# Kernel tuning notes

Hardware: AMD Instinct MI355X
Metric: run time of the kernel (lower is better)

Reference implementation:

```python
import jax, jax.numpy as jnp
import numpy as np

D_MODEL = 1024
N_HEADS = 16
HEAD_DIM = D_MODEL // N_HEADS
WINDOW = 512


def _rope(q, k, seq_len, head_dim):
    # interleaved RoPE, identical to the torch implementation
    theta = 1.0 / 10000.0 ** (jnp.arange(0, head_dim, 2, dtype=jnp.float32) / head_dim)
    pos = jnp.arange(seq_len, dtype=jnp.float32)
    freqs = jnp.outer(pos, theta)                      # [S, hD/2]
    cos_f = jnp.cos(freqs)[None, None]                 # [1,1,S,hD/2]
    sin_f = jnp.sin(freqs)[None, None]

    def rotate(x):
        x1, x2 = x[..., ::2], x[..., 1::2]
        return jnp.stack([x1 * cos_f - x2 * sin_f, x1 * sin_f + x2 * cos_f], axis=-1).reshape(x.shape)

    return rotate(q), rotate(k)


def _sliding_window_attn(q, k, v, W, scale):
    # chunked O(S*W) causal sliding-window attention
    B, nH, S, hD = q.shape
    n_chunks = (S + W - 1) // W
    pad_s = n_chunks * W - S
    k_pad = jnp.pad(k, ((0, 0), (0, 0), (W, pad_s), (0, 0)))
    v_pad = jnp.pad(v, ((0, 0), (0, 0), (W, pad_s), (0, 0)))
    q_pad = jnp.pad(q, ((0, 0), (0, 0), (0, pad_s), (0, 0)))
    q_c = q_pad.reshape(B, nH, n_chunks, W, hD)
    k_r = k_pad.reshape(B, nH, n_chunks + 1, W, hD)
    v_r = v_pad.reshape(B, nH, n_chunks + 1, W, hD)
    # window i = chunks [i, i+1] of the left-padded sequence (== torch unfold)
    k_c = jnp.concatenate([k_r[:, :, :-1], k_r[:, :, 1:]], axis=3)  # [B,nH,C,2W,hD]
    v_c = jnp.concatenate([v_r[:, :, :-1], v_r[:, :, 1:]], axis=3)
    attn = jnp.einsum('bhcqd,bhckd->bhcqk', q_c, k_c) * scale

    qi = jnp.arange(W)[:, None]
    ki = jnp.arange(2 * W)[None, :]
    cw_mask = (ki <= qi) | (ki > qi + W)               # [W, 2W]
    chunk_idx = jnp.arange(n_chunks)[:, None]
    abs_k = chunk_idx * W + ki - W                     # [C, 2W]
    pad_mask = (abs_k < 0) | (abs_k >= S)
    q_pos = jnp.arange(n_chunks * W).reshape(n_chunks, W)
    full_mask = cw_mask[None] | pad_mask[:, None, :] | (q_pos >= S)[..., None]  # [C,W,2W]

    attn = jnp.where(full_mask[None, None], -jnp.inf, attn)
    attn = jax.nn.softmax(attn, axis=-1)
    attn = jnp.nan_to_num(attn, nan=0.0)
    out = jnp.einsum('bhcqk,bhckd->bhcqd', attn, v_c)
    return out.reshape(B, nH, n_chunks * W, hD)[:, :, :S]


def _rmsnorm(x, w):
    eps = jnp.finfo(x.dtype).eps
    return x * jax.lax.rsqrt(jnp.mean(x * x, axis=-1, keepdims=True) + eps) * w


def _sdpa(q, k, v, scale):
    s = jnp.einsum('bhqd,bhkd->bhqk', q, k) * scale
    return jnp.einsum('bhqk,bhkd->bhqd', jax.nn.softmax(s, axis=-1), v)


def setup_inputs() -> dict:
    key = jax.random.key(0)
    ks = jax.random.split(key, 11)
    D = D_MODEL
    std = 0.02
    return {
        'x': jax.random.normal(ks[0], (2, 4096, D), jnp.float32),
        'landmarks': jax.random.normal(ks[1], (2, 256, D), jnp.float32),
        'archived_landmarks': jax.random.normal(ks[2], (2, 128, D), jnp.float32),
        'W_qkv': jax.random.normal(ks[3], (D, 3 * D), jnp.float32) * std,
        'W_lm': jax.random.normal(ks[4], (D, 2 * D), jnp.float32) * std,
        'W_arch': jax.random.normal(ks[5], (D, 2 * D), jnp.float32) * std,
        'W_o': jax.random.normal(ks[6], (D, D), jnp.float32) * std,
        'W_gate': jax.random.normal(ks[7], (3 * D, 2 * D), jnp.float32) * std,
        'g_local': jnp.ones((D,), jnp.float32),
        'g_lm': jnp.ones((D,), jnp.float32),
        'g_arch': jnp.ones((D,), jnp.float32),
    }


def reference(x, landmarks, archived_landmarks, W_qkv, W_lm, W_arch, W_o, W_gate, g_local, g_lm, g_arch):
    B, S, D = x.shape
    nH, hD = N_HEADS, HEAD_DIM
    scale = hD ** -0.5

    def rsh(t, L):
        return jnp.transpose(t.reshape(B, L, nH, hD), (0, 2, 1, 3))

    q, k, v = jnp.split(x @ W_qkv, 3, axis=-1)
    Q, K, V = rsh(q, S), rsh(k, S), rsh(v, S)
    Q, K = _rope(Q, K, S, hD)

    Weff = min(WINDOW, S)
    out_loc = _sliding_window_attn(Q, K, V, Weff, scale)  # S > Weff -> chunked path
    out_loc = _rmsnorm(jnp.transpose(out_loc, (0, 2, 1, 3)).reshape(B, S, D), g_local)

    L = landmarks.shape[1]
    K_lm, V_lm = jnp.split(landmarks @ W_lm, 2, axis=-1)
    out_lm = _sdpa(Q, rsh(K_lm, L), rsh(V_lm, L), scale)
    out_lm = _rmsnorm(jnp.transpose(out_lm, (0, 2, 1, 3)).reshape(B, S, D), g_lm)

    A = archived_landmarks.shape[1]
    K_a, V_a = jnp.split(archived_landmarks @ W_arch, 2, axis=-1)
    out_a = _sdpa(Q, rsh(K_a, A), rsh(V_a, A), scale)
    out_a = _rmsnorm(jnp.transpose(out_a, (0, 2, 1, 3)).reshape(B, S, D), g_arch)

    concat = jnp.concatenate([out_loc, out_lm, out_a], axis=-1)
    gate, value = jnp.split(concat @ W_gate, 2, axis=-1)
    return (jax.nn.silu(gate) * value) @ W_o
```

## Files before the change

kernel.cpp:

```cpp
#include <hip/hip_runtime.h>
#include <cstdint>
#include <cstddef>

typedef __bf16 bf16;
typedef __bf16 bf16x2 __attribute__((ext_vector_type(2)));
typedef __bf16 bf16x4 __attribute__((ext_vector_type(4)));
typedef __bf16 bf16x8 __attribute__((ext_vector_type(8)));
typedef float  f32x2 __attribute__((ext_vector_type(2)));
typedef float  f32x4 __attribute__((ext_vector_type(4)));

#define DEVFN __device__ __forceinline__

DEVFN void gld_lds16(void* lds, const void* g) {
  __builtin_amdgcn_global_load_lds(
      (__attribute__((address_space(1))) void*)g,
      (__attribute__((address_space(3))) void*)lds,
      16, 0, 0);
}

__global__ void cast_f32_bf16(const float* __restrict__ in, bf16* __restrict__ out, int n4) {
  int i = blockIdx.x * blockDim.x + threadIdx.x;
  if (i < n4) {
    f32x4 v = reinterpret_cast<const f32x4*>(in)[i];
    bf16x4 o;
    o[0] = (bf16)v[0]; o[1] = (bf16)v[1]; o[2] = (bf16)v[2]; o[3] = (bf16)v[3];
    reinterpret_cast<bf16x4*>(out)[i] = o;
  }
}

__global__ void transpose_cast(const float* __restrict__ in, bf16* __restrict__ out,
                               int R, int C) {
  __shared__ float t[32][33];
  int tx = threadIdx.x, ty = threadIdx.y;
  int c = blockIdx.x * 32 + tx;
  #pragma unroll
  for (int j = 0; j < 4; ++j) {
    int r = blockIdx.y * 32 + ty + j * 8;
    t[ty + j * 8][tx] = in[(size_t)r * C + c];
  }
  __syncthreads();
  int rr = blockIdx.y * 32 + tx;
  #pragma unroll
  for (int j = 0; j < 4; ++j) {
    int cc = blockIdx.x * 32 + ty + j * 8;
    out[(size_t)cc * R + rr] = (bf16)t[tx][ty + j * 8];
  }
}

__global__ void rope_table(float* __restrict__ tab) {
  int idx = blockIdx.x * 256 + threadIdx.x;
  int s = idx >> 5, i = idx & 31;
  float theta = powf(10000.f, -(float)(2 * i) * (1.f / 64.f));
  float f = (float)s * theta;
  tab[idx * 2]     = cosf(f);
  tab[idx * 2 + 1] = sinf(f);
}

template<typename OT>
__global__ __launch_bounds__(256) void gemm_bf16(
    const bf16* __restrict__ A, const bf16* __restrict__ Bt, OT* __restrict__ C,
    int M, int N, int K) {
  __shared__ alignas(16) bf16 As[128 * 64];
  __shared__ alignas(16) bf16 Bs[128 * 64];
  int tid = threadIdx.x;
  int w = tid >> 6, l = tid & 63;
  int l15 = l & 15, lg = l >> 4;
  int m0 = blockIdx.y * 128;
  int n0 = blockIdx.x * 128;
  int wr = (w >> 1) * 64, wc = (w & 1) * 64;
  f32x4 acc[4][4] = {};
  const size_t aBase = (size_t)m0 * K;
  const size_t bBase = (size_t)n0 * K;
  int nk = K >> 6;
  for (int kt = 0; kt < nk; ++kt) {
    int k0 = kt << 6;
    #pragma unroll
    for (int it = 0; it < 4; ++it) {
      int c = it * 256 + tid;
      int row = c >> 3, c8 = c & 7;
      gld_lds16(&As[(size_t)(it * 256 + w * 64) * 8],
                A + aBase + (size_t)row * K + k0 + c8 * 8);
      gld_lds16(&Bs[(size_t)(it * 256 + w * 64) * 8],
                Bt + bBase + (size_t)row * K + k0 + c8 * 8);
    }
    __syncthreads();
    #pragma unroll
    for (int kk = 0; kk < 64; kk += 32) {
      bf16x8 a[4], b[4];
      #pragma unroll
      for (int i = 0; i < 4; ++i)
        a[i] = *reinterpret_cast<const bf16x8*>(&As[(wr + i * 16 + l15) * 64 + kk + lg * 8]);
      #pragma unroll
      for (int i = 0; i < 4; ++i)
        b[i] = *reinterpret_cast<const bf16x8*>(&Bs[(wc + i * 16 + l15) * 64 + kk + lg * 8]);
      #pragma unroll
      for (int mi = 0; mi < 4; ++mi)
        #pragma unroll
        for (int ni = 0; ni < 4; ++ni)
          acc[mi][ni] = __builtin_amdgcn_mfma_f32_16x16x32_bf16(a[mi], b[ni], acc[mi][ni], 0, 0, 0);
    }
    __syncthreads();
  }
  #pragma unroll
  for (int mi = 0; mi < 4; ++mi) {
    #pragma unroll
    for (int r = 0; r < 4; ++r) {
      int row = m0 + wr + mi * 16 + lg * 4 + r;
      OT* crow = C + (size_t)row * N + n0 + wc + l15;
      #pragma unroll
      for (int ni = 0; ni < 4; ++ni) crow[ni * 16] = (OT)acc[mi][ni][r];
    }
  }
}

__global__ void rope_qk(const bf16* __restrict__ qkv, const float* __restrict__ tab,
                        bf16* __restrict__ Qb, bf16* __restrict__ Kb) {
  int idx = blockIdx.x * 256 + threadIdx.x;
  int i = idx & 31;
  int h = (idx >> 5) & 15;
  int bs = idx >> 9;
  int s = bs & 4095;
  int b = bs >> 12;
  const bf16* row = qkv + (size_t)bs * 3072;
  bf16x2 q2 = *reinterpret_cast<const bf16x2*>(row + h * 64 + 2 * i);
  bf16x2 k2 = *reinterpret_cast<const bf16x2*>(row + 1024 + h * 64 + 2 * i);
  f32x2 cs = *reinterpret_cast<const f32x2*>(tab + s * 64 + 2 * i);
  float c = cs[0], sn = cs[1];
  float q0 = (float)q2[0], q1 = (float)q2[1];
  float k0 = (float)k2[0], k1 = (float)k2[1];
  size_t ob = (((size_t)(b * 16 + h) * 4096) + s) * 64 + 2 * i;
  bf16x2 qo, ko;
  qo[0] = (bf16)((q0 * c - q1 * sn) * 0.125f);
  qo[1] = (bf16)((q0 * sn + q1 * c) * 0.125f);
  ko[0] = (bf16)(k0 * c - k1 * sn);
  ko[1] = (bf16)(k0 * sn + k1 * c);
  *reinterpret_cast<bf16x2*>(Qb + ob) = qo;
  *reinterpret_cast<bf16x2*>(Kb + ob) = ko;
}

__global__ void kv_post(const bf16* __restrict__ kv, bf16* __restrict__ Kdst,
                        bf16* __restrict__ Vt, int Lk, int rs, int koff, int voff) {
  __shared__ float t[64][65];
  int s0 = blockIdx.x * 64;
  int h = blockIdx.y, b = blockIdx.z;
  int tid = threadIdx.x;
  int lane_d = tid & 63;
  int rq = tid >> 6;
  const bf16* base = kv + (size_t)b * Lk * rs;
  if (Kdst) {
    #pragma unroll
    for (int r = 0; r < 16; ++r) {
      int si = r * 4 + rq;
      Kdst[(((size_t)(b * 16 + h) * Lk) + s0 + si) * 64 + lane_d] =
          base[(size_t)(s0 + si) * rs + koff + h * 64 + lane_d];
    }
  }
  #pragma unroll
  for (int r = 0; r < 16; ++r) {
    int si = r * 4 + rq;
    t[si][lane_d] = (float)base[(size_t)(s0 + si) * rs + voff + h * 64 + lane_d];
  }
  __syncthreads();
  #pragma unroll
  for (int r = 0; r < 16; ++r) {
    int d = r * 4 + rq;
    Vt[(((size_t)(b * 16 + h) * 64) + d) * Lk + s0 + lane_d] = (bf16)t[lane_d][d];
  }
}

template<bool WINDOWED>
__global__ __launch_bounds__(256) void attn_kernel(
    const bf16* __restrict__ Qb, const bf16* __restrict__ Kb, const bf16* __restrict__ Vt,
    bf16* __restrict__ outc, int S, int Lk, int col_off) {
  __shared__ alignas(16) bf16 Ks[64 * 64];
  __shared__ alignas(16) bf16 Vs[64 * 64];
  __shared__ alignas(16) bf16 Ps[4][16 * 72];
  int tid = threadIdx.x;
  int w = tid >> 6, l = tid & 63;
  int l15 = l & 15, lg = l >> 4;
  int qt = blockIdx.x, h = blockIdx.y, b = blockIdx.z;

  size_t qrow = (((size_t)(b * 16 + h) * S) + qt * 64 + w * 16 + l15) * 64;
  bf16x8 qf[2];
  qf[0] = *reinterpret_cast<const bf16x8*>(Qb + qrow + lg * 8);
  qf[1] = *reinterpret_cast<const bf16x8*>(Qb + qrow + 32 + lg * 8);
  const bf16* Kbase = Kb + ((size_t)(b * 16 + h) * Lk) * 64;
  const bf16* Vbase = Vt + ((size_t)(b * 16 + h) * 64) * Lk;

  float mrow = -1e30f, lsum = 0.f;
  f32x4 acc[4] = {};

  int kt_hi, kt_lo;
  if (WINDOWED) { kt_hi = qt; kt_lo = qt >= 8 ? qt - 8 : 0; }
  else          { kt_hi = (Lk >> 6) - 1; kt_lo = 0; }

  for (int kt = kt_hi; kt >= kt_lo; --kt) {
    const bf16* kg = Kbase + (size_t)kt * 64 * 64;
    #pragma unroll
    for (int it = 0; it < 2; ++it)
      gld_lds16(&Ks[(it * 256 + w * 64) * 8], kg + (size_t)(it * 256 + tid) * 8);
    #pragma unroll
    for (int it = 0; it < 2; ++it) {
      int c = it * 256 + tid;
      int row = c >> 3, c8 = c & 7;
      gld_lds16(&Vs[(it * 256 + w * 64) * 8],
                Vbase + (size_t)row * Lk + kt * 64 + c8 * 8);
    }
    __syncthreads();

    f32x4 st[4] = {};
    #pragma unroll
    for (int kk = 0; kk < 2; ++kk) {
      #pragma unroll
      for (int f = 0; f < 4; ++f) {
        bf16x8 kf = *reinterpret_cast<const bf16x8*>(&Ks[(f * 16 + l15) * 64 + kk * 32 + lg * 8]);
        st[f] = __builtin_amdgcn_mfma_f32_16x16x32_bf16(kf, qf[kk], st[f], 0, 0, 0);
      }
    }

    if (WINDOWED) {
      int qi = w * 16 + l15;
      if (kt == qt) {
        #pragma unroll
        for (int f = 0; f < 4; ++f)
          #pragma unroll
          for (int r = 0; r < 4; ++r)
            if (f * 16 + lg * 4 + r > qi) st[f][r] = -1e30f;
      } else if (kt == qt - 8) {
        #pragma unroll
        for (int f = 0; f < 4; ++f)
          #pragma unroll
          for (int r = 0; r < 4; ++r)
            if (f * 16 + lg * 4 + r <= qi) st[f][r] = -1e30f;
      }
    }

    float rm = -1e30f;
    #pragma unroll
    for (int f = 0; f < 4; ++f)
      #pragma unroll
      for (int r = 0; r < 4; ++r) rm = fmaxf(rm, st[f][r]);
    rm = fmaxf(rm, __shfl_xor(rm, 16));
    rm = fmaxf(rm, __shfl_xor(rm, 32));
    float mnew = fmaxf(mrow, rm);
    float fsc = __expf(mrow - mnew);
    float ps = 0.f;
    bf16x4 pv[4];
    #pragma unroll
    for (int f = 0; f < 4; ++f)
      #pragma unroll
      for (int r = 0; r < 4; ++r) {
        float p = __expf(st[f][r] - mnew);
        ps += p;
        pv[f][r] = (bf16)p;
      }
    ps += __shfl_xor(ps, 16);
    ps += __shfl_xor(ps, 32);
    lsum = lsum * fsc + ps;
    mrow = mnew;

    #pragma unroll
    for (int f = 0; f < 4; ++f)
      *reinterpret_cast<bf16x4*>(&Ps[w][l15 * 72 + f * 16 + lg * 4]) = pv[f];

    #pragma unroll
    for (int r = 0; r < 4; ++r) {
      float fr = __shfl(fsc, lg * 4 + r);
      #pragma unroll
      for (int f = 0; f < 4; ++f) acc[f][r] *= fr;
    }

    #pragma unroll
    for (int kk = 0; kk < 2; ++kk) {
      bf16x8 pa = *reinterpret_cast<const bf16x8*>(&Ps[w][l15 * 72 + kk * 32 + lg * 8]);
      #pragma unroll
      for (int f = 0; f < 4; ++f) {
        bf16x8 vf = *reinterpret_cast<const bf16x8*>(&Vs[(f * 16 + l15) * 64 + kk * 32 + lg * 8]);
        acc[f] = __builtin_amdgcn_mfma_f32_16x16x32_bf16(pa, vf, acc[f], 0, 0, 0);
      }
    }
    __syncthreads();
  }

  float inv = 1.f / lsum;
  #pragma unroll
  for (int r = 0; r < 4; ++r) {
    float ir = __shfl(inv, lg * 4 + r);
    int srow = qt * 64 + w * 16 + lg * 4 + r;
    bf16* orow = outc + ((size_t)b * S + srow) * 3072 + col_off + h * 64 + l15;
    #pragma unroll
    for (int f = 0; f < 4; ++f) orow[f * 16] = (bf16)(acc[f][r] * ir);
  }
}

__global__ __launch_bounds__(256) void rmsnorm_kernel(
    bf16* data, const float* __restrict__ g0,
    const float* __restrict__ g1, const float* __restrict__ g2) {
  int token = blockIdx.x;
  int seg = blockIdx.y;
  const float* g = seg == 0 ? g0 : (seg == 1 ? g1 : g2);
  int tid = threadIdx.x;
  size_t base = (size_t)token * 3072 + seg * 1024;
  bf16x4 bv = reinterpret_cast<const bf16x4*>(data + base)[tid];
  f32x4 v;
  #pragma unroll
  for (int j = 0; j < 4; ++j) v[j] = (float)bv[j];
  float ss = v[0] * v[0] + v[1] * v[1] + v[2] * v[2] + v[3] * v[3];
  #pragma unroll
  for (int m = 1; m < 64; m <<= 1) ss += __shfl_xor(ss, m);
  __shared__ float red[4];
  if ((tid & 63) == 0) red[tid >> 6] = ss;
  __syncthreads();
  float tot = red[0] + red[1] + red[2] + red[3];
  float sc = rsqrtf(tot * (1.f / 1024.f) + 1.19209290e-07f);
  f32x4 gv = reinterpret_cast<const f32x4*>(g)[tid];
  bf16x4 o;
  #pragma unroll
  for (int j = 0; j < 4; ++j) o[j] = (bf16)(v[j] * sc * gv[j]);
  reinterpret_cast<bf16x4*>(data + base)[tid] = o;
}

__global__ void silu_kernel(const bf16* __restrict__ gv, bf16* __restrict__ out) {
  int T = blockIdx.x * 256 + threadIdx.x;
  int row = T >> 8, c4 = (T & 255) * 4;
  bf16x4 g = *reinterpret_cast<const bf16x4*>(gv + (size_t)row * 2048 + c4);
  bf16x4 vv = *reinterpret_cast<const bf16x4*>(gv + (size_t)row * 2048 + 1024 + c4);
  bf16x4 o;
  #pragma unroll
  for (int j = 0; j < 4; ++j) {
    float x = (float)g[j];
    o[j] = (bf16)((x / (1.f + __expf(-x))) * (float)vv[j]);
  }
  *reinterpret_cast<bf16x4*>(out + (size_t)row * 1024 + c4) = o;
}

extern "C" void kernel_launch(void* const* d_in, const int* in_sizes, int n_in,
                              void* d_out, int out_size, void* d_ws, size_t ws_size,
                              hipStream_t stream) {
  (void)in_sizes; (void)n_in; (void)out_size; (void)ws_size;
  const float* x       = (const float*)d_in[0];
  const float* lm      = (const float*)d_in[1];
  const float* arch    = (const float*)d_in[2];
  const float* W_qkv   = (const float*)d_in[3];
  const float* W_lm    = (const float*)d_in[4];
  const float* W_arch  = (const float*)d_in[5];
  const float* W_o     = (const float*)d_in[6];
  const float* W_gate  = (const float*)d_in[7];
  const float* g_local = (const float*)d_in[8];
  const float* g_lm    = (const float*)d_in[9];
  const float* g_arch  = (const float*)d_in[10];
  float* out = (float*)d_out;

  char* ws = (char*)d_ws;
  size_t off = 0;
  auto alloc = [&](size_t bytes) -> void* {
    void* p = ws + off;
    off += (bytes + 255) & ~(size_t)255;
    return p;
  };
  bf16*  Wqkv_t   = (bf16*) alloc(3072ull * 1024 * 2);
  bf16*  Wlm_t    = (bf16*) alloc(2048ull * 1024 * 2);
  bf16*  Warch_t  = (bf16*) alloc(2048ull * 1024 * 2);
  bf16*  Wgate_t  = (bf16*) alloc(2048ull * 3072 * 2);
  bf16*  Wo_t     = (bf16*) alloc(1024ull * 1024 * 2);
  bf16*  lm_bf    = (bf16*) alloc(512ull * 1024 * 2);
  bf16*  arch_bf  = (bf16*) alloc(256ull * 1024 * 2);
  float* ropetab  = (float*)alloc(4096ull * 64 * 4);
  bf16*  Klm      = (bf16*) alloc(2ull * 16 * 256 * 64 * 2);
  bf16*  Vlm_t    = (bf16*) alloc(2ull * 16 * 64 * 256 * 2);
  bf16*  Ka       = (bf16*) alloc(2ull * 16 * 128 * 64 * 2);
  bf16*  Va_t     = (bf16*) alloc(2ull * 16 * 64 * 128 * 2);
  bf16*  lmkv_bf  = (bf16*) alloc(512ull * 2048 * 2);
  bf16*  akv_bf   = (bf16*) alloc(256ull * 2048 * 2);
  char* R1 = (char*)alloc(8192ull * 1024 * 2);
  bf16* x_bf  = (bf16*)R1;
  bf16* gated = (bf16*)R1;
  char* R2 = (char*)alloc(8192ull * 3072 * 2);
  bf16* qkv_bf  = (bf16*)R2;
  bf16* concatb = (bf16*)R2;
  char* R3 = (char*)alloc(3ull * 16 * 1024 * 1024);
  bf16* Qb = (bf16*)R3;
  bf16* Kb = (bf16*)(R3 + 16ull * 1024 * 1024);
  bf16* Vt = (bf16*)(R3 + 32ull * 1024 * 1024);
  bf16* gv = (bf16*)R3;

  transpose_cast<<<dim3(96, 32), dim3(32, 8), 0, stream>>>(W_qkv, Wqkv_t, 1024, 3072);
  transpose_cast<<<dim3(64, 32), dim3(32, 8), 0, stream>>>(W_lm, Wlm_t, 1024, 2048);
  transpose_cast<<<dim3(64, 32), dim3(32, 8), 0, stream>>>(W_arch, Warch_t, 1024, 2048);
  transpose_cast<<<dim3(64, 96), dim3(32, 8), 0, stream>>>(W_gate, Wgate_t, 3072, 2048);
  transpose_cast<<<dim3(32, 32), dim3(32, 8), 0, stream>>>(W_o, Wo_t, 1024, 1024);
  cast_f32_bf16<<<8192, 256, 0, stream>>>(x, x_bf, 8192 * 1024 / 4);
  cast_f32_bf16<<<512, 256, 0, stream>>>(lm, lm_bf, 512 * 1024 / 4);
  cast_f32_bf16<<<256, 256, 0, stream>>>(arch, arch_bf, 256 * 1024 / 4);
  rope_table<<<512, 256, 0, stream>>>(ropetab);

  gemm_bf16<bf16><<<dim3(24, 64), 256, 0, stream>>>(x_bf, Wqkv_t, qkv_bf, 8192, 3072, 1024);
  gemm_bf16<bf16><<<dim3(16, 4), 256, 0, stream>>>(lm_bf, Wlm_t, lmkv_bf, 512, 2048, 1024);
  gemm_bf16<bf16><<<dim3(16, 2), 256, 0, stream>>>(arch_bf, Warch_t, akv_bf, 256, 2048, 1024);

  rope_qk<<<16384, 256, 0, stream>>>(qkv_bf, ropetab, Qb, Kb);
  kv_post<<<dim3(64, 16, 2), 256, 0, stream>>>(qkv_bf, nullptr, Vt, 4096, 3072, 0, 2048);
  kv_post<<<dim3(4, 16, 2), 256, 0, stream>>>(lmkv_bf, Klm, Vlm_t, 256, 2048, 0, 1024);
  kv_post<<<dim3(2, 16, 2), 256, 0, stream>>>(akv_bf, Ka, Va_t, 128, 2048, 0, 1024);

  attn_kernel<true><<<dim3(64, 16, 2), 256, 0, stream>>>(Qb, Kb, Vt, concatb, 4096, 4096, 0);
  attn_kernel<false><<<dim3(64, 16, 2), 256, 0, stream>>>(Qb, Klm, Vlm_t, concatb, 4096, 256, 1024);
  attn_kernel<false><<<dim3(64, 16, 2), 256, 0, stream>>>(Qb, Ka, Va_t, concatb, 4096, 128, 2048);

  rmsnorm_kernel<<<dim3(8192, 3), 256, 0, stream>>>(concatb, g_local, g_lm, g_arch);

  gemm_bf16<bf16><<<dim3(16, 64), 256, 0, stream>>>(concatb, Wgate_t, gv, 8192, 2048, 3072);
  silu_kernel<<<8192, 256, 0, stream>>>(gv, gated);
  gemm_bf16<float><<<dim3(8, 64), 256, 0, stream>>>(gated, Wo_t, out, 8192, 1024, 1024);
}
```

Before: 490.1 us.

## Add 256x256-tile GEMM with 8 waves, double-buffered LDS and XCD swizzle

Adds a new GEMM kernel that uses 256x256 output tiles, 512 threads and double-buffered LDS fed by direct global-to-LDS loads with an XOR swizzle. It interleaves MFMA blocks with next-tile staging, uses s_setprio and explicit barriers, and remaps block IDs across the 8 XCDs. The large QKV, gate and output projections are switched to this kernel. The aim is more data reuse per tile and more overlap of memory loads with compute. The trade-off is fewer workgroups (128 for the output projection, fewer than the CU count) and a higher register load from the 8x4 accumulators.

```diff
diff --git a/kernel.cpp b/kernel.cpp
--- a/kernel.cpp
+++ b/kernel.cpp
@@ -10,6 +10,8 @@
 typedef float  f32x4 __attribute__((ext_vector_type(4)));
 
 #define DEVFN __device__ __forceinline__
+#define BAR()  asm volatile("s_barrier" ::: "memory")
+#define VMW4() asm volatile("s_waitcnt vmcnt(4)" ::: "memory")
 
 DEVFN void gld_lds16(void* lds, const void* g) {
   __builtin_amdgcn_global_load_lds(
@@ -54,6 +56,121 @@
   float f = (float)s * theta;
   tab[idx * 2]     = cosf(f);
   tab[idx * 2 + 1] = sinf(f);
+}
+
+template<typename OT>
+__global__ __launch_bounds__(512) void gemm256(
+    const bf16* __restrict__ A, const bf16* __restrict__ Bt, OT* __restrict__ C,
+    int M, int N, int K) {
+  __shared__ alignas(16) bf16 lds[2][2][2][256 * 32];
+  const int tid = threadIdx.x;
+  const int w = tid >> 6, l = tid & 63;
+  const int l15 = l & 15, lg = l >> 4;
+  const int wm = w >> 2, wn = w & 3;
+  const int nwg = gridDim.x, qx = nwg >> 3;
+  const int swz = (blockIdx.x & 7) * qx + (blockIdx.x >> 3);
+  const int gx = N >> 8;
+  const int m0 = (swz / gx) << 8;
+  const int n0 = (swz % gx) << 8;
+  const int nt = K >> 6;
+
+  auto stage = [&](int b, int ab, int kk, int t) {
+    const bf16* __restrict__ src = ab ? Bt : A;
+    const int base0 = ab ? n0 : m0;
+    const int k0 = (t << 6) + (kk << 5);
+    #pragma unroll
+    for (int i = 0; i < 2; ++i) {
+      int u = i * 512 + tid;
+      int row = u >> 2, slot = u & 3;
+      int sslot = slot ^ ((row >> 1) & 3);
+      gld_lds16(&lds[b][ab][kk][(i * 512 + w * 64) * 8],
+                src + (size_t)(base0 + row) * K + k0 + sslot * 8);
+    }
+  };
+  auto rd = [&](int b, int ab, int kk, int r) -> bf16x8 {
+    return *reinterpret_cast<const bf16x8*>(
+        &lds[b][ab][kk][(r << 5) + ((lg ^ ((r >> 1) & 3)) << 3)]);
+  };
+
+  f32x4 acc[8][4] = {};
+  bf16x8 afr[4], bfr[4];
+
+  stage(0, 0, 0, 0);
+  stage(0, 1, 0, 0);
+  stage(0, 0, 1, 0);
+  stage(0, 1, 1, 0);
+  VMW4();
+  BAR();
+
+  for (int t = 0; t < nt; ++t) {
+    const int c = t & 1;
+    const bool st = (t + 1) < nt;
+    #pragma unroll
+    for (int f = 0; f < 4; ++f) afr[f] = rd(c, 0, 0, wm * 128 + f * 16 + l15);
+    #pragma unroll
+    for (int f = 0; f < 4; ++f) bfr[f] = rd(c, 1, 0, wn * 64 + f * 16 + l15);
+    if (st) stage(c ^ 1, 0, 0, t + 1);
+    BAR();
+    __builtin_amdgcn_s_setprio(1);
+    #pragma unroll
+    for (int mi = 0; mi < 4; ++mi)
+      #pragma unroll
+      for (int ni = 0; ni < 4; ++ni)
+        acc[mi][ni] = __builtin_amdgcn_mfma_f32_16x16x32_bf16(afr[mi], bfr[ni], acc[mi][ni], 0, 0, 0);
+    __builtin_amdgcn_s_setprio(0);
+    BAR();
+    #pragma unroll
+    for (int f = 0; f < 4; ++f) afr[f] = rd(c, 0, 0, wm * 128 + (f + 4) * 16 + l15);
+    if (st) stage(c ^ 1, 1, 0, t + 1);
+    BAR();
+    __builtin_amdgcn_s_setprio(1);
+    #pragma unroll
+    for (int mi = 0; mi < 4; ++mi)
+      #pragma unroll
+      for (int ni = 0; ni < 4; ++ni)
+        acc[mi + 4][ni] = __builtin_amdgcn_mfma_f32_16x16x32_bf16(afr[mi], bfr[ni], acc[mi + 4][ni], 0, 0, 0);
+    __builtin_amdgcn_s_setprio(0);
+    VMW4();
+    BAR();
+    #pragma unroll
+    for (int f = 0; f < 4; ++f) afr[f] = rd(c, 0, 1, wm * 128 + f * 16 + l15);
+    #pragma unroll
+    for (int f = 0; f < 4; ++f) bfr[f] = rd(c, 1, 1, wn * 64 + f * 16 + l15);
+    if (st) stage(c ^ 1, 0, 1, t + 1);
+    BAR();
+    __builtin_amdgcn_s_setprio(1);
+    #pragma unroll
+    for (int mi = 0; mi < 4; ++mi)
+      #pragma unroll
+      for (int ni = 0; ni < 4; ++ni)
+        acc[mi][ni] = __builtin_amdgcn_mfma_f32_16x16x32_bf16(afr[mi], bfr[ni], acc[mi][ni], 0, 0, 0);
+    __builtin_amdgcn_s_setprio(0);
+    BAR();
+    #pragma unroll
+    for (int f = 0; f < 4; ++f) afr[f] = rd(c, 0, 1, wm * 128 + (f + 4) * 16 + l15);
+    if (st) stage(c ^ 1, 1, 1, t + 1);
+    BAR();
+    __builtin_amdgcn_s_setprio(1);
+    #pragma unroll
+    for (int mi = 0; mi < 4; ++mi)
+      #pragma unroll
+      for (int ni = 0; ni < 4; ++ni)
+        acc[mi + 4][ni] = __builtin_amdgcn_mfma_f32_16x16x32_bf16(afr[mi], bfr[ni], acc[mi + 4][ni], 0, 0, 0);
+    __builtin_amdgcn_s_setprio(0);
+    VMW4();
+    BAR();
+  }
+
+  #pragma unroll
+  for (int mi = 0; mi < 8; ++mi) {
+    #pragma unroll
+    for (int r = 0; r < 4; ++r) {
+      int row = m0 + wm * 128 + mi * 16 + lg * 4 + r;
+      OT* crow = C + (size_t)row * N + n0 + wn * 64 + l15;
+      #pragma unroll
+      for (int ni = 0; ni < 4; ++ni) crow[ni * 16] = (OT)acc[mi][ni][r];
+    }
+  }
 }
 
 template<typename OT>
@@ -394,7 +511,7 @@
   cast_f32_bf16<<<256, 256, 0, stream>>>(arch, arch_bf, 256 * 1024 / 4);
   rope_table<<<512, 256, 0, stream>>>(ropetab);
 
-  gemm_bf16<bf16><<<dim3(24, 64), 256, 0, stream>>>(x_bf, Wqkv_t, qkv_bf, 8192, 3072, 1024);
+  gemm256<bf16><<<32 * 12, 512, 0, stream>>>(x_bf, Wqkv_t, qkv_bf, 8192, 3072, 1024);
   gemm_bf16<bf16><<<dim3(16, 4), 256, 0, stream>>>(lm_bf, Wlm_t, lmkv_bf, 512, 2048, 1024);
   gemm_bf16<bf16><<<dim3(16, 2), 256, 0, stream>>>(arch_bf, Warch_t, akv_bf, 256, 2048, 1024);
 
@@ -409,7 +526,7 @@
 
   rmsnorm_kernel<<<dim3(8192, 3), 256, 0, stream>>>(concatb, g_local, g_lm, g_arch);
 
-  gemm_bf16<bf16><<<dim3(16, 64), 256, 0, stream>>>(concatb, Wgate_t, gv, 8192, 2048, 3072);
+  gemm256<bf16><<<32 * 8, 512, 0, stream>>>(concatb, Wgate_t, gv, 8192, 2048, 3072);
   silu_kernel<<<8192, 256, 0, stream>>>(gv, gated);
-  gemm_bf16<float><<<dim3(8, 64), 256, 0, stream>>>(gated, Wo_t, out, 8192, 1024, 1024);
-}
+  gemm256<float><<<32 * 4, 512, 0, stream>>>(gated, Wo_t, out, 8192, 1024, 1024);
+}
```

Measured after the change: 436.3 us. 11.0% less time.
